# Kernel tuning notes

Measured on AMD Instinct MI355X. Metric: run time of the kernel, lower is better.

## Reference

```python
import jax, jax.numpy as jnp
import numpy as np

NEG_SLOPE = 0.01  # nn.LeakyReLU default


def setup_inputs() -> dict:
    key = jax.random.key(0)
    k1, k2, k3 = jax.random.split(key, 3)
    N, F_IN, F_OUT = 8192, 128, 64
    h = jax.random.normal(k1, (N, F_IN), dtype=jnp.float32)
    W = jax.random.normal(k2, (F_IN, F_OUT), dtype=jnp.float32) * (1.414 / np.sqrt(F_IN))
    a = jax.random.normal(k3, (2 * F_OUT, 1), dtype=jnp.float32) * (1.414 / np.sqrt(2 * F_OUT))
    return {"h": h, "W": W, "a": a}


def reference(h, W, a):
    # Wh: [N, F_out]
    Wh = h @ W
    F_out = W.shape[1]
    a1 = a[:F_out, 0]   # applies to the "source" (row) node i
    a2 = a[F_out:, 0]   # applies to the "target" (col) node j
    # e[i, j] = leakyrelu(a1 . Wh_i + a2 . Wh_j)  -- algebraic decomposition of
    # the concat-based score; avoids the O(N^2 * 2F) concat tensor.
    f1 = Wh @ a1  # [N]
    f2 = Wh @ a2  # [N]
    e = jax.nn.leaky_relu(f1[:, None] + f2[None, :], negative_slope=NEG_SLOPE)  # [N, N]
    attention = jax.nn.softmax(e, axis=1)
    # dropout is identity in eval mode (training=False)
    h_prime = attention @ Wh  # [N, F_out]
    return jax.nn.elu(h_prime)  # concat=True branch
```

## Files before the change

### kernel.cpp

```cpp
#include <hip/hip_runtime.h>
#include <hip/hip_bf16.h>
#include <stdint.h>

typedef float f32x4 __attribute__((ext_vector_type(4)));
typedef short s16x8 __attribute__((ext_vector_type(8)));
typedef short s16x4 __attribute__((ext_vector_type(4)));
typedef unsigned int u32x4 __attribute__((ext_vector_type(4)));

#define L2E 1.44269504088896f

__device__ __forceinline__ float bf2f(unsigned short u) {
    return __uint_as_float(((unsigned int)u) << 16);
}
__device__ __forceinline__ unsigned short f2bf_rne(float f) {
    unsigned int u = __float_as_uint(f);
    u += 0x7fffu + ((u >> 16) & 1u);
    return (unsigned short)(u >> 16);
}

__global__ __launch_bounds__(256) void k1_wh(
    const float* __restrict__ hf,
    const float* __restrict__ Wf,
    const float* __restrict__ af,
    unsigned short* __restrict__ whB,
    float* __restrict__ g1L,
    float* __restrict__ g2L,
    float* __restrict__ E1L,
    float* __restrict__ E2L)
{
    __shared__ __align__(16) unsigned short Wt[64][136];
    __shared__ __align__(16) unsigned short tb[64][72];
    const int tid  = threadIdx.x;
    const int lane = tid & 63;
    const int w    = tid >> 6;
    const int col  = lane & 15;
    const int quad = lane >> 4;
    const int i0   = blockIdx.x * 64;

    #pragma unroll
    for (int it = 0; it < 8; ++it) {
        int fidx = tid + it * 256;
        int k  = fidx >> 4;
        int n4 = (fidx & 15) << 2;
        f32x4 wv = *(const f32x4*)&Wf[k * 64 + n4];
        #pragma unroll
        for (int e = 0; e < 4; ++e)
            Wt[n4 + e][k] = f2bf_rne(wv[e]);
    }
    __syncthreads();

    f32x4 D[4];
    #pragma unroll
    for (int f = 0; f < 4; ++f) D[f] = (f32x4){0.f, 0.f, 0.f, 0.f};

    const int rowA = i0 + w * 16 + col;
    #pragma unroll
    for (int cs = 0; cs < 4; ++cs) {
        f32x4 h0 = *(const f32x4*)&hf[(size_t)rowA * 128 + cs * 32 + quad * 8];
        f32x4 h1 = *(const f32x4*)&hf[(size_t)rowA * 128 + cs * 32 + quad * 8 + 4];
        s16x8 A;
        #pragma unroll
        for (int jj = 0; jj < 4; ++jj) {
            A[jj]     = (short)f2bf_rne(h0[jj]);
            A[4 + jj] = (short)f2bf_rne(h1[jj]);
        }
        #pragma unroll
        for (int f = 0; f < 4; ++f) {
            s16x8 B = *(const s16x8*)&Wt[f * 16 + col][cs * 32 + quad * 8];
            D[f] = __builtin_amdgcn_mfma_f32_16x16x32_bf16(A, B, D[f], 0, 0, 0);
        }
    }

    float a1v[4], a2v[4];
    #pragma unroll
    for (int f = 0; f < 4; ++f) {
        a1v[f] = af[f * 16 + col];
        a2v[f] = af[64 + f * 16 + col];
    }

    #pragma unroll
    for (int r = 0; r < 4; ++r) {
        float s1 = D[0][r]*a1v[0] + D[1][r]*a1v[1] + D[2][r]*a1v[2] + D[3][r]*a1v[3];
        float s2 = D[0][r]*a2v[0] + D[1][r]*a2v[1] + D[2][r]*a2v[2] + D[3][r]*a2v[3];
        #pragma unroll
        for (int d = 1; d < 16; d <<= 1) {
            s1 += __shfl_xor(s1, d, 64);
            s2 += __shfl_xor(s2, d, 64);
        }
        if (col == 0) {
            int i = i0 + w * 16 + quad * 4 + r;
            g1L[i] = __builtin_amdgcn_exp2f(s1 * L2E);
            g2L[i] = __builtin_amdgcn_exp2f(s1 * (0.01f * L2E));
            E1L[i] = __builtin_amdgcn_exp2f(s2 * L2E);
            E2L[i] = __builtin_amdgcn_exp2f(s2 * (0.01f * L2E));
        }
        #pragma unroll
        for (int f = 0; f < 4; ++f)
            tb[f * 16 + col][w * 16 + quad * 4 + r] = f2bf_rne(D[f][r]);
    }
    __syncthreads();

    for (int idx = tid; idx < 512; idx += 256) {
        int lane_o = idx & 63;
        int bq     = (idx >> 6) & 3;
        int jg_l   = idx >> 8;
        int col_o  = lane_o & 15, quad_o = lane_o >> 4;
        u32x4 v = *(const u32x4*)&tb[bq * 16 + col_o][jg_l * 32 + quad_o * 8];
        size_t off = (((size_t)((i0 >> 5) + jg_l) * 4 + bq) * 64 + lane_o) * 8;
        *(u32x4*)&whB[off] = v;
    }
}

__global__ __launch_bounds__(512, 4) void k2_attn(
    const unsigned short* __restrict__ whB,
    const float* __restrict__ g1L,
    const float* __restrict__ g2L,
    const float* __restrict__ E1L,
    const float* __restrict__ E2L,
    unsigned short* __restrict__ Apart,
    float* __restrict__ rsumP)
{
    __shared__ __align__(16) unsigned short BtF[16384];
    __shared__ __align__(16) float E1s[256];
    __shared__ __align__(16) float E2s[256];
    const int tid  = threadIdx.x;
    const int lane = tid & 63;
    const int w    = tid >> 6;
    const int col  = lane & 15;
    const int quad = lane >> 4;
    const int i0   = blockIdx.x * 128;
    const int jb   = blockIdx.y * 1024;

    const float g1 = g1L[i0 + w * 16 + col];
    const float g2 = g2L[i0 + w * 16 + col];

    f32x4 D0 = (f32x4){0.f,0.f,0.f,0.f}, D1 = D0, D2 = D0, D3 = D0, Ds = D0;
    s16x8 ones;
    #pragma unroll
    for (int jj = 0; jj < 8; ++jj) ones[jj] = (short)0x3f80;

    for (int s = 0; s < 4; ++s) {
        __syncthreads();
        if (tid < 64)
            *(f32x4*)&E1s[tid * 4] = *(const f32x4*)&E1L[jb + (s << 8) + tid * 4];
        else if (tid < 128) {
            int t = tid - 64;
            *(f32x4*)&E2s[t * 4] = *(const f32x4*)&E2L[jb + (s << 8) + t * 4];
        }
        {
            const unsigned short* src = whB + ((size_t)(jb >> 5) + s * 8) * 2048;
            #pragma unroll
            for (int it = 0; it < 4; ++it) {
                int idx = (tid + it * 512) * 8;
                *(u32x4*)&BtF[idx] = *(const u32x4*)&src[idx];
            }
        }
        __syncthreads();
        #pragma unroll
        for (int j0 = 0; j0 < 256; j0 += 32) {
            const int jq = j0 + quad * 8;
            f32x4 ea1 = *(const f32x4*)&E1s[jq];
            f32x4 eb1 = *(const f32x4*)&E1s[jq + 4];
            f32x4 ea2 = *(const f32x4*)&E2s[jq];
            f32x4 eb2 = *(const f32x4*)&E2s[jq + 4];
            unsigned int pb[8];
            #pragma unroll
            for (int e = 0; e < 4; ++e) {
                pb[e]     = __float_as_uint(fmaxf(g1 * ea1[e], g2 * ea2[e]));
                pb[4 + e] = __float_as_uint(fmaxf(g1 * eb1[e], g2 * eb2[e]));
            }
            union { u32x4 u4; s16x8 s8; } Au;
            Au.u4[0] = __builtin_amdgcn_perm(pb[1], pb[0], 0x07060302u);
            Au.u4[1] = __builtin_amdgcn_perm(pb[3], pb[2], 0x07060302u);
            Au.u4[2] = __builtin_amdgcn_perm(pb[5], pb[4], 0x07060302u);
            Au.u4[3] = __builtin_amdgcn_perm(pb[7], pb[6], 0x07060302u);
            const unsigned short* bf = &BtF[(size_t)(j0 >> 5) * 2048 + lane * 8];
            s16x8 B0 = *(const s16x8*)(bf);
            s16x8 B1 = *(const s16x8*)(bf + 512);
            s16x8 B2 = *(const s16x8*)(bf + 1024);
            s16x8 B3 = *(const s16x8*)(bf + 1536);
            D0 = __builtin_amdgcn_mfma_f32_16x16x32_bf16(Au.s8, B0, D0, 0, 0, 0);
            D1 = __builtin_amdgcn_mfma_f32_16x16x32_bf16(Au.s8, B1, D1, 0, 0, 0);
            D2 = __builtin_amdgcn_mfma_f32_16x16x32_bf16(Au.s8, B2, D2, 0, 0, 0);
            D3 = __builtin_amdgcn_mfma_f32_16x16x32_bf16(Au.s8, B3, D3, 0, 0, 0);
            Ds = __builtin_amdgcn_mfma_f32_16x16x32_bf16(Au.s8, ones, Ds, 0, 0, 0);
        }
    }

    unsigned short* Ap = Apart + (size_t)blockIdx.y * 524288;
    #pragma unroll
    for (int r = 0; r < 4; ++r) {
        int i = i0 + w * 16 + quad * 4 + r;
        Ap[(size_t)i * 64 +      col] = f2bf_rne(D0[r]);
        Ap[(size_t)i * 64 + 16 + col] = f2bf_rne(D1[r]);
        Ap[(size_t)i * 64 + 32 + col] = f2bf_rne(D2[r]);
        Ap[(size_t)i * 64 + 48 + col] = f2bf_rne(D3[r]);
        if (col == 0) rsumP[blockIdx.y * 8192 + i] = Ds[r];
    }
}

__global__ __launch_bounds__(256) void k3_combine(
    const unsigned short* __restrict__ Apart,
    const float* __restrict__ rsumP,
    float* __restrict__ out)
{
    int gid = blockIdx.x * 256 + threadIdx.x;
    int i  = gid >> 4;
    int c4 = (gid & 15) << 2;
    f32x4 num = (f32x4){0.f, 0.f, 0.f, 0.f};
    float den = 0.f;
    #pragma unroll
    for (int s = 0; s < 8; ++s) {
        s16x4 pv = *(const s16x4*)&Apart[(size_t)s * 524288 + (size_t)i * 64 + c4];
        #pragma unroll
        for (int e = 0; e < 4; ++e) num[e] += bf2f((unsigned short)pv[e]);
        den += rsumP[s * 8192 + i];
    }
    float rden = 1.f / den;
    f32x4 o;
    #pragma unroll
    for (int e = 0; e < 4; ++e) {
        float v = num[e] * rden;
        o[e] = v > 0.f ? v : (__builtin_amdgcn_exp2f(v * L2E) - 1.f);
    }
    *(f32x4*)&out[(size_t)i * 64 + c4] = o;
}

extern "C" void kernel_launch(void* const* d_in, const int* in_sizes, int n_in,
                              void* d_out, int out_size, void* d_ws, size_t ws_size,
                              hipStream_t stream) {
    const float* h = (const float*)d_in[0];
    const float* W = (const float*)d_in[1];
    const float* a = (const float*)d_in[2];
    float* out = (float*)d_out;

    char* ws = (char*)d_ws;
    unsigned short* whB   = (unsigned short*)ws;
    float* g1L            = (float*)(ws + 1048576);
    float* g2L            = (float*)(ws + 1081344);
    float* E1L            = (float*)(ws + 1114112);
    float* E2L            = (float*)(ws + 1146880);
    unsigned short* Apart = (unsigned short*)(ws + 1179648);
    float* rsumP          = (float*)(ws + 9568256);

    k1_wh<<<128, 256, 0, stream>>>(h, W, a, whB, g1L, g2L, E1L, E2L);
    k2_attn<<<dim3(64, 8), 512, 0, stream>>>(whB, g1L, g2L, E1L, E2L, Apart, rsumP);
    k3_combine<<<512, 256, 0, stream>>>(Apart, rsumP, out);
}
```

Measured before the change: 83.46 us.

## Split attention j-range across wave halves so each B fragment feeds two row tiles

The k2_attn kernel now gives each wave two 16-row tiles and half of the j-steps, where before it had one row tile and every j-step. Each B fragment loaded from LDS then feeds two sets of MFMAs, halving B LDS reads per MFMA and doubling the independent accumulator chains. The two wave halves combine their partial accumulators through shared memory at the end, which adds a reduction pass, an extra barrier and more accumulator registers that could lower occupancy.

```diff
diff --git a/kernel.cpp b/kernel.cpp
--- a/kernel.cpp
+++ b/kernel.cpp
@@ -126,15 +126,20 @@
     const int tid  = threadIdx.x;
     const int lane = tid & 63;
     const int w    = tid >> 6;
+    const int rg   = w & 3;
+    const int jh   = w >> 2;
     const int col  = lane & 15;
     const int quad = lane >> 4;
     const int i0   = blockIdx.x * 128;
     const int jb   = blockIdx.y * 1024;
 
-    const float g1 = g1L[i0 + w * 16 + col];
-    const float g2 = g2L[i0 + w * 16 + col];
-
-    f32x4 D0 = (f32x4){0.f,0.f,0.f,0.f}, D1 = D0, D2 = D0, D3 = D0, Ds = D0;
+    const float g1a = g1L[i0 + rg * 16 + col];
+    const float g2a = g2L[i0 + rg * 16 + col];
+    const float g1b = g1L[i0 + (rg + 4) * 16 + col];
+    const float g2b = g2L[i0 + (rg + 4) * 16 + col];
+
+    f32x4 Da0 = (f32x4){0.f,0.f,0.f,0.f}, Da1 = Da0, Da2 = Da0, Da3 = Da0, Dsa = Da0;
+    f32x4 Db0 = Da0, Db1 = Da0, Db2 = Da0, Db3 = Da0, Dsb = Da0;
     s16x8 ones;
     #pragma unroll
     for (int jj = 0; jj < 8; ++jj) ones[jj] = (short)0x3f80;
@@ -157,45 +162,91 @@
         }
         __syncthreads();
         #pragma unroll
-        for (int j0 = 0; j0 < 256; j0 += 32) {
+        for (int t = 0; t < 4; ++t) {
+            const int j0 = jh * 32 + t * 64;
             const int jq = j0 + quad * 8;
             f32x4 ea1 = *(const f32x4*)&E1s[jq];
             f32x4 eb1 = *(const f32x4*)&E1s[jq + 4];
             f32x4 ea2 = *(const f32x4*)&E2s[jq];
             f32x4 eb2 = *(const f32x4*)&E2s[jq + 4];
-            unsigned int pb[8];
+            unsigned int pa[8], pb[8];
             #pragma unroll
             for (int e = 0; e < 4; ++e) {
-                pb[e]     = __float_as_uint(fmaxf(g1 * ea1[e], g2 * ea2[e]));
-                pb[4 + e] = __float_as_uint(fmaxf(g1 * eb1[e], g2 * eb2[e]));
+                pa[e]     = __float_as_uint(fmaxf(g1a * ea1[e], g2a * ea2[e]));
+                pa[4 + e] = __float_as_uint(fmaxf(g1a * eb1[e], g2a * eb2[e]));
+                pb[e]     = __float_as_uint(fmaxf(g1b * ea1[e], g2b * ea2[e]));
+                pb[4 + e] = __float_as_uint(fmaxf(g1b * eb1[e], g2b * eb2[e]));
             }
-            union { u32x4 u4; s16x8 s8; } Au;
-            Au.u4[0] = __builtin_amdgcn_perm(pb[1], pb[0], 0x07060302u);
-            Au.u4[1] = __builtin_amdgcn_perm(pb[3], pb[2], 0x07060302u);
-            Au.u4[2] = __builtin_amdgcn_perm(pb[5], pb[4], 0x07060302u);
-            Au.u4[3] = __builtin_amdgcn_perm(pb[7], pb[6], 0x07060302u);
+            union { u32x4 u4; s16x8 s8; } Aa, Ab;
+            Aa.u4[0] = __builtin_amdgcn_perm(pa[1], pa[0], 0x07060302u);
+            Aa.u4[1] = __builtin_amdgcn_perm(pa[3], pa[2], 0x07060302u);
+            Aa.u4[2] = __builtin_amdgcn_perm(pa[5], pa[4], 0x07060302u);
+            Aa.u4[3] = __builtin_amdgcn_perm(pa[7], pa[6], 0x07060302u);
+            Ab.u4[0] = __builtin_amdgcn_perm(pb[1], pb[0], 0x07060302u);
+            Ab.u4[1] = __builtin_amdgcn_perm(pb[3], pb[2], 0x07060302u);
+            Ab.u4[2] = __builtin_amdgcn_perm(pb[5], pb[4], 0x07060302u);
+            Ab.u4[3] = __builtin_amdgcn_perm(pb[7], pb[6], 0x07060302u);
             const unsigned short* bf = &BtF[(size_t)(j0 >> 5) * 2048 + lane * 8];
             s16x8 B0 = *(const s16x8*)(bf);
             s16x8 B1 = *(const s16x8*)(bf + 512);
             s16x8 B2 = *(const s16x8*)(bf + 1024);
             s16x8 B3 = *(const s16x8*)(bf + 1536);
-            D0 = __builtin_amdgcn_mfma_f32_16x16x32_bf16(Au.s8, B0, D0, 0, 0, 0);
-            D1 = __builtin_amdgcn_mfma_f32_16x16x32_bf16(Au.s8, B1, D1, 0, 0, 0);
-            D2 = __builtin_amdgcn_mfma_f32_16x16x32_bf16(Au.s8, B2, D2, 0, 0, 0);
-            D3 = __builtin_amdgcn_mfma_f32_16x16x32_bf16(Au.s8, B3, D3, 0, 0, 0);
-            Ds = __builtin_amdgcn_mfma_f32_16x16x32_bf16(Au.s8, ones, Ds, 0, 0, 0);
-        }
-    }
-
-    unsigned short* Ap = Apart + (size_t)blockIdx.y * 524288;
-    #pragma unroll
-    for (int r = 0; r < 4; ++r) {
-        int i = i0 + w * 16 + quad * 4 + r;
-        Ap[(size_t)i * 64 +      col] = f2bf_rne(D0[r]);
-        Ap[(size_t)i * 64 + 16 + col] = f2bf_rne(D1[r]);
-        Ap[(size_t)i * 64 + 32 + col] = f2bf_rne(D2[r]);
-        Ap[(size_t)i * 64 + 48 + col] = f2bf_rne(D3[r]);
-        if (col == 0) rsumP[blockIdx.y * 8192 + i] = Ds[r];
+            Da0 = __builtin_amdgcn_mfma_f32_16x16x32_bf16(Aa.s8, B0, Da0, 0, 0, 0);
+            Da1 = __builtin_amdgcn_mfma_f32_16x16x32_bf16(Aa.s8, B1, Da1, 0, 0, 0);
+            Da2 = __builtin_amdgcn_mfma_f32_16x16x32_bf16(Aa.s8, B2, Da2, 0, 0, 0);
+            Da3 = __builtin_amdgcn_mfma_f32_16x16x32_bf16(Aa.s8, B3, Da3, 0, 0, 0);
+            Dsa = __builtin_amdgcn_mfma_f32_16x16x32_bf16(Aa.s8, ones, Dsa, 0, 0, 0);
+            Db0 = __builtin_amdgcn_mfma_f32_16x16x32_bf16(Ab.s8, B0, Db0, 0, 0, 0);
+            Db1 = __builtin_amdgcn_mfma_f32_16x16x32_bf16(Ab.s8, B1, Db1, 0, 0, 0);
+            Db2 = __builtin_amdgcn_mfma_f32_16x16x32_bf16(Ab.s8, B2, Db2, 0, 0, 0);
+            Db3 = __builtin_amdgcn_mfma_f32_16x16x32_bf16(Ab.s8, B3, Db3, 0, 0, 0);
+            Dsb = __builtin_amdgcn_mfma_f32_16x16x32_bf16(Ab.s8, ones, Dsb, 0, 0, 0);
+        }
+    }
+
+    __syncthreads();
+    float* Cf = (float*)BtF;
+    float* Sf = E1s;
+    if (jh == 1) {
+        #pragma unroll
+        for (int r = 0; r < 4; ++r) {
+            int ra = (rg * 16 + quad * 4 + r) * 64;
+            int rb = ((rg + 4) * 16 + quad * 4 + r) * 64;
+            Cf[ra +      col] = Da0[r];
+            Cf[ra + 16 + col] = Da1[r];
+            Cf[ra + 32 + col] = Da2[r];
+            Cf[ra + 48 + col] = Da3[r];
+            Cf[rb +      col] = Db0[r];
+            Cf[rb + 16 + col] = Db1[r];
+            Cf[rb + 32 + col] = Db2[r];
+            Cf[rb + 48 + col] = Db3[r];
+            if (col == 0) {
+                Sf[rg * 16 + quad * 4 + r]       = Dsa[r];
+                Sf[(rg + 4) * 16 + quad * 4 + r] = Dsb[r];
+            }
+        }
+    }
+    __syncthreads();
+    if (jh == 0) {
+        unsigned short* Ap = Apart + (size_t)blockIdx.y * 524288;
+        #pragma unroll
+        for (int r = 0; r < 4; ++r) {
+            int la = rg * 16 + quad * 4 + r;
+            int lb = (rg + 4) * 16 + quad * 4 + r;
+            int ia = i0 + la, ib = i0 + lb;
+            Ap[(size_t)ia * 64 +      col] = f2bf_rne(Da0[r] + Cf[la * 64 +      col]);
+            Ap[(size_t)ia * 64 + 16 + col] = f2bf_rne(Da1[r] + Cf[la * 64 + 16 + col]);
+            Ap[(size_t)ia * 64 + 32 + col] = f2bf_rne(Da2[r] + Cf[la * 64 + 32 + col]);
+            Ap[(size_t)ia * 64 + 48 + col] = f2bf_rne(Da3[r] + Cf[la * 64 + 48 + col]);
+            Ap[(size_t)ib * 64 +      col] = f2bf_rne(Db0[r] + Cf[lb * 64 +      col]);
+            Ap[(size_t)ib * 64 + 16 + col] = f2bf_rne(Db1[r] + Cf[lb * 64 + 16 + col]);
+            Ap[(size_t)ib * 64 + 32 + col] = f2bf_rne(Db2[r] + Cf[lb * 64 + 32 + col]);
+            Ap[(size_t)ib * 64 + 48 + col] = f2bf_rne(Db3[r] + Cf[lb * 64 + 48 + col]);
+            if (col == 0) {
+                rsumP[blockIdx.y * 8192 + ia] = Dsa[r] + Sf[la];
+                rsumP[blockIdx.y * 8192 + ib] = Dsb[r] + Sf[lb];
+            }
+        }
     }
 }
 
```

New measurement: 83.75 us. Within noise of the previous version (+0.3%).
